# Kernel optimization log

Measured on AMD Instinct MI355X. Metric: run time of the kernel, lower is better.

The kernel has to match this reference:

```python
import jax, jax.numpy as jnp
import numpy as np

B, T, C = 32, 400, 3000
SN, SD = 128, 512   # numerator / denominator FSM state counts
NEG = -1e4          # log-zero surrogate (finite for grad safety)
DEN_SCALE = 1.0
DO_AVG = False


def setup_inputs() -> dict:
    key = jax.random.key(0)
    ks = jax.random.split(key, 8)
    x = jax.random.normal(ks[0], (B, T, C), jnp.float32)
    seqlengths = jax.random.randint(ks[1], (B,), T // 2, T + 1)
    # Numerator FSMs: batched left-to-right chains with self-loops.
    i = np.arange(SN)
    band = (i[None, :] >= i[:, None]) & (i[None, :] - i[:, None] <= 1)
    num_trans = jnp.where(jnp.asarray(band),
                          0.1 * jax.random.normal(ks[2], (B, SN, SN), jnp.float32), NEG)
    num_pdf = jax.random.randint(ks[3], (B, SN), 0, C)
    num_init = jnp.broadcast_to(jnp.where(jnp.arange(SN) == 0, 0.0, NEG), (B, SN)).astype(jnp.float32)
    num_final = jnp.broadcast_to(jnp.where(jnp.arange(SN) == SN - 1, 0.0, NEG), (B, SN)).astype(jnp.float32)
    # Denominator FSM: one dense graph shared by the whole batch.
    den_trans = 0.1 * jax.random.normal(ks[4], (SD, SD), jnp.float32)
    den_pdf = jax.random.randint(ks[5], (SD,), 0, C)
    den_init = 0.1 * jax.random.normal(ks[6], (SD,), jnp.float32)
    den_final = 0.1 * jax.random.normal(ks[7], (SD,), jnp.float32)
    return dict(input=x, seqlengths=seqlengths,
                num_trans=num_trans, num_pdf=num_pdf, num_init=num_init, num_final=num_final,
                den_trans=den_trans, den_pdf=den_pdf, den_init=den_init, den_final=den_final)


def _log_marginal(ll, seqlengths, trans, pdf, init, final):
    """FSM forward recursion in the log domain.
    ll: [B,T,C]; trans: [B,S,S] or [S,S]; pdf/init/final: [B,S].
    Returns per-sequence log-marginal [B]."""
    Bn, Tn, _ = ll.shape
    S = pdf.shape[-1]
    # Per-state emissions: em[b,t,s] = ll[b,t,pdf[b,s]]
    em = jnp.take_along_axis(ll, jnp.broadcast_to(pdf[:, None, :], (Bn, Tn, S)), axis=2)
    alpha0 = init + em[:, 0]                              # [B,S]
    mask = jnp.arange(1, Tn)[:, None] < seqlengths[None, :]  # [T-1,B]

    def step(alpha, xs):
        em_t, m = xs
        new = jax.nn.logsumexp(alpha[:, :, None] + trans, axis=1) + em_t
        return jnp.where(m[:, None], new, alpha), None

    alphaT, _ = jax.lax.scan(step, alpha0, (jnp.swapaxes(em, 0, 1)[1:], mask))
    return jax.nn.logsumexp(alphaT + final, axis=-1)      # [B]


def reference(input, seqlengths, num_trans, num_pdf, num_init, num_final,
              den_trans, den_pdf, den_init, den_final):
    ll = jnp.clip(input, -30.0, 30.0)
    Bn = ll.shape[0]
    num_llh = _log_marginal(ll, seqlengths, num_trans, num_pdf, num_init, num_final).sum()
    den_llh = _log_marginal(
        ll, seqlengths, den_trans,
        jnp.broadcast_to(den_pdf[None], (Bn, SD)),
        jnp.broadcast_to(den_init[None], (Bn, SD)),
        jnp.broadcast_to(den_final[None], (Bn, SD))).sum()
    loss = -(num_llh - DEN_SCALE * den_llh)
    if DO_AVG:
        loss = loss / seqlengths.sum()
    return loss
```

## Files before the change

### kernel.cpp

```cpp
#include <hip/hip_runtime.h>

#define B_ 32
#define T_ 400
#define C_ 3000
#define SN_ 128
#define SD_ 512
#define LN120 4.78749174f
#define LNU 2.70805020f
#define SPANB 48

__device__ __forceinline__ float clip30(float v) { return fminf(30.f, fmaxf(-30.f, v)); }

__device__ __forceinline__ int dot8u4(unsigned a, unsigned b, int c) {
#if __has_builtin(__builtin_amdgcn_udot8)
    return (int)__builtin_amdgcn_udot8(a, b, (unsigned)c, false);
#else
    int r = c;
    #pragma unroll
    for (int i = 0; i < 8; ++i)
        r += (int)((a >> (4 * i)) & 0xF) * (int)((b >> (4 * i)) & 0xF);
    return r;
#endif
}

template <int CTRL>
__device__ __forceinline__ int dpp_i(int v) {
    return __builtin_amdgcn_update_dpp(v, v, CTRL, 0xF, 0xF, false);
}
template <int CTRL>
__device__ __forceinline__ float fmaxdpp(float v) {
    int mv = __builtin_amdgcn_update_dpp(__float_as_int(v), __float_as_int(v), CTRL, 0xF, 0xF, false);
    return fmaxf(v, __int_as_float(mv));
}
template <int CTRL>
__device__ __forceinline__ float faddpp(float v) {
    int mv = __builtin_amdgcn_update_dpp(__float_as_int(v), __float_as_int(v), CTRL, 0xF, 0xF, false);
    return v + __int_as_float(mv);
}
template <int CTRL>
__device__ __forceinline__ float fxaddf(float a, float b) {
    int t = __builtin_amdgcn_update_dpp(__float_as_int(b), __float_as_int(b), CTRL, 0xF, 0xF, false);
    return a + __int_as_float(t);
}
__device__ __forceinline__ float swz16f(float v) {
    return __int_as_float(__builtin_amdgcn_ds_swizzle(__float_as_int(v), 0x401F));
}
__device__ __forceinline__ float wavemax_fast(float v) {
    v = fmaxdpp<0x121>(v); v = fmaxdpp<0x122>(v);
    v = fmaxdpp<0x124>(v); v = fmaxdpp<0x128>(v);
    float a = __int_as_float(__builtin_amdgcn_readlane(__float_as_int(v), 0));
    float b = __int_as_float(__builtin_amdgcn_readlane(__float_as_int(v), 16));
    float c = __int_as_float(__builtin_amdgcn_readlane(__float_as_int(v), 32));
    float d = __int_as_float(__builtin_amdgcn_readlane(__float_as_int(v), 48));
    return fmaxf(fmaxf(a, b), fmaxf(c, d));
}
__device__ __forceinline__ float waveallsum(float v) {
    v = faddpp<0x121>(v); v = faddpp<0x122>(v);
    v = faddpp<0x124>(v); v = faddpp<0x128>(v);
    v = v + swz16f(v);
    v = v + __shfl_xor(v, 32, 64);
    return v;
}
__device__ __forceinline__ void barrier_lds() {
    asm volatile("s_waitcnt lgkmcnt(0)\n\ts_barrier" ::: "memory");
}

__global__ void prep(const float* __restrict__ dt, unsigned* __restrict__ tp8,
                     const float* __restrict__ x, const int* __restrict__ den_pdf,
                     const int* __restrict__ num_pdf,
                     float* __restrict__ em_den, float* __restrict__ em_num) {
    size_t id = (size_t)blockIdx.x * 1024 + threadIdx.x;
    if (id < 32768) {
        int o = (int)id;
        int b4 = o & 3, tid = (o >> 2) & 511, k = o >> 11;
        int r = 4 * k + b4;
        int m = r >> 3, i = r & 7;
        int g = tid >> 3, j = tid & 7;
        int s_out = 8 * g + (m ^ j);
        int src0 = 64 * j + 8 * i;
        unsigned wv = 0;
        #pragma unroll
        for (int nb = 0; nb < 8; ++nb) {
            float e = __expf(dt[(src0 + nb) * SD_ + s_out]);
            int pq = __float2int_rn(e * 8.f);
            if (pq > 15) pq = 15;
            wv |= (unsigned)pq << (4 * nb);
        }
        tp8[o] = wv;
    } else if (id < 32768 + 6553600) {
        size_t e = id - 32768;
        int s = (int)(e & 511);
        size_t bt = e >> 9;
        em_den[e] = __expf(clip30(x[bt * C_ + den_pdf[s]]));
    } else if (id < 32768 + 6553600 + 1638400) {
        size_t e = id - 32768 - 6553600;
        int s = (int)(e & 127);
        size_t bt = e >> 7;
        int b = (int)(bt / 400);
        em_num[e] = clip30(x[bt * C_ + num_pdf[b * SN_ + s]]);
    }
}

__global__ __launch_bounds__(512, 1)
void fwd_kernel(const int* __restrict__ seqlen,
                const float* __restrict__ num_trans,
                const float* __restrict__ num_init, const float* __restrict__ num_final,
                const unsigned* __restrict__ tp8,
                const float* __restrict__ den_init, const float* __restrict__ den_final,
                const float* __restrict__ em_den, const float* __restrict__ em_num,
                float* __restrict__ parts) {
    const int tid = threadIdx.x;

    if (blockIdx.x < B_) {
        __shared__ __align__(16) unsigned char ea[2][8 * SPANB];
        __shared__ float Ms[2][8];
        __shared__ float fr[8];
        const int b = blockIdx.x;
        const int L = seqlen[b];
        const int w = tid >> 6, l = tid & 63;
        const int j = tid & 7;

        unsigned tq[64];
        {
            const uint4* tg = (const uint4*)tp8;
            #pragma unroll
            for (int i = 0; i < 16; ++i) {
                uint4 v = tg[(i << 9) + tid];
                tq[4 * i + 0] = v.x;
                tq[4 * i + 1] = v.y;
                tq[4 * i + 2] = v.z;
                tq[4 * i + 3] = v.w;
            }
        }

        const float* emp = em_den + (size_t)b * T_ * SD_ + tid;

        #define NPACK(UN, BUF) { \
            int uu = (UN); \
            uu |= dpp_i<0xB1>(uu) << 4; \
            uu |= dpp_i<0x4E>(uu) << 8; \
            uu |= dpp_i<0x124>(uu) << 16; \
            if ((tid & 7) == 0) \
                *(unsigned*)&ea[(BUF)][SPANB * w + ((tid & 63) >> 1)] = (unsigned)uu; }

        float a0lin = __expf(den_init[tid]) * emp[0];
        float K0 = wavemax_fast(a0lin);
        int un = __float2int_rn(15.f * a0lin * __builtin_amdgcn_rcpf(K0));
        float ms_w = __logf(K0);
        NPACK(un, 0)
        if (l == 0) Ms[0][w] = ms_w;
        barrier_lds();

        float EA = emp[SD_], EB = emp[2 * SD_];
        int cur = 0;
        for (int t = 1; t < L; ++t) {
            int tn = (t + 2 < L) ? t + 2 : L - 1;
            float EN = emp[(size_t)tn * SD_];

            float ms_j = Ms[cur][j];
            const uint4* er = (const uint4*)&ea[cur][SPANB * j];
            uint4 e0 = er[0], e1 = er[1];

            int ac0, ac1, ac2, ac3, ac4, ac5, ac6, ac7;
            #define DOTD0(W, I) \
                ac0 = dot8u4((W), tq[(I)],      0); \
                ac1 = dot8u4((W), tq[8 + (I)],  0); \
                ac2 = dot8u4((W), tq[16 + (I)], 0); \
                ac3 = dot8u4((W), tq[24 + (I)], 0); \
                ac4 = dot8u4((W), tq[32 + (I)], 0); \
                ac5 = dot8u4((W), tq[40 + (I)], 0); \
                ac6 = dot8u4((W), tq[48 + (I)], 0); \
                ac7 = dot8u4((W), tq[56 + (I)], 0);
            #define DOTD(W, I) \
                ac0 = dot8u4((W), tq[(I)],      ac0); \
                ac1 = dot8u4((W), tq[8 + (I)],  ac1); \
                ac2 = dot8u4((W), tq[16 + (I)], ac2); \
                ac3 = dot8u4((W), tq[24 + (I)], ac3); \
                ac4 = dot8u4((W), tq[32 + (I)], ac4); \
                ac5 = dot8u4((W), tq[40 + (I)], ac5); \
                ac6 = dot8u4((W), tq[48 + (I)], ac6); \
                ac7 = dot8u4((W), tq[56 + (I)], ac7);
            DOTD0(e0.x, 0) DOTD(e0.y, 1) DOTD(e0.z, 2) DOTD(e0.w, 3)
            DOTD(e1.x, 4)  DOTD(e1.y, 5) DOTD(e1.z, 6) DOTD(e1.w, 7)
            #undef DOTD
            #undef DOTD0

            float e_own = __expf(ms_j - ms_w);
            float f0 = (float)ac0 * e_own, f1 = (float)ac1 * e_own;
            float f2 = (float)ac2 * e_own, f3 = (float)ac3 * e_own;
            float f4 = (float)ac4 * e_own, f5 = (float)ac5 * e_own;
            float f6 = (float)ac6 * e_own, f7 = (float)ac7 * e_own;
            f0 = fxaddf<0xB1>(f0, f1);  f2 = fxaddf<0xB1>(f2, f3);
            f4 = fxaddf<0xB1>(f4, f5);  f6 = fxaddf<0xB1>(f6, f7);
            f0 = fxaddf<0x4E>(f0, f2);  f4 = fxaddf<0x4E>(f4, f6);
            f0 = fxaddf<0x124>(f0, f4);

            float Kv = f0 * EA;
            float K = wavemax_fast(Kv);
            un = __float2int_rn(15.f * Kv * __builtin_amdgcn_rcpf(K));
            NPACK(un, cur ^ 1)
            ms_w = ms_w + __logf(K) - LN120;
            if (l == 0) Ms[cur ^ 1][w] = ms_w;
            EA = EB; EB = EN;
            barrier_lds();
            cur ^= 1;
        }
        #undef NPACK

        float mm = Ms[cur][0];
        #pragma unroll
        for (int k2 = 1; k2 < 8; ++k2) mm = fmaxf(mm, Ms[cur][k2]);
        float fv = (float)un * __expf(den_final[tid] + (ms_w - mm));
        fv = waveallsum(fv);
        if (l == 0) fr[w] = fv;
        __syncthreads();
        if (tid == 0) {
            float tot = 0.f;
            for (int i = 0; i < 8; ++i) tot += fr[i];
            parts[B_ + b] = mm + __logf(tot) - LNU;
        }
    } else {
        __shared__ float aLn[2][4][SN_];
        __shared__ float nredn[4][2];
        const int nb = blockIdx.x - B_;
        const int lb = tid >> 7;
        const int b  = nb * 4 + lb;
        const int s  = tid & 127;
        const int L  = seqlen[b];
        const int lane = tid & 63;
        const int wv2 = (tid >> 6) & 1;
        const float* ep = em_num + (size_t)b * T_ * SN_ + s;
        const float tself = num_trans[((size_t)b * SN_ + s) * SN_ + s];
        const float tup = (s > 0) ? num_trans[((size_t)b * SN_ + (s - 1)) * SN_ + s] : 0.f;
        float alpha = num_init[b * SN_ + s] + ep[0];
        aLn[0][lb][s] = alpha;
        __syncthreads();
        float emA = ep[SN_], emB = ep[2 * SN_];
        int cur = 0;
        for (int t = 1; t < T_; ++t) {
            int tt = t + 2; if (tt > T_ - 1) tt = T_ - 1;
            float emN = ep[(size_t)tt * SN_];
            bool live = (t < L);
            float yy = alpha + tself;
            float newa;
            if (s > 0) {
                float xx = aLn[cur][lb][s - 1] + tup;
                float mx = fmaxf(xx, yy), mn = fminf(xx, yy);
                newa = mx + log1pf(__expf(mn - mx)) + emA;
            } else {
                newa = yy + emA;
            }
            if (live) alpha = newa;
            aLn[cur ^ 1][lb][s] = alpha;
            emA = emB; emB = emN;
            __syncthreads();
            cur ^= 1;
        }
        float v = alpha + num_final[b * SN_ + s];
        float wm = v;
        #pragma unroll
        for (int o = 32; o; o >>= 1) wm = fmaxf(wm, __shfl_xor(wm, o, 64));
        if (lane == 0) nredn[lb][wv2] = wm;
        __syncthreads();
        float fm = fmaxf(nredn[lb][0], nredn[lb][1]);
        __syncthreads();
        float pe = __expf(v - fm);
        #pragma unroll
        for (int o = 32; o; o >>= 1) pe += __shfl_xor(pe, o, 64);
        if (lane == 0) nredn[lb][wv2] = pe;
        __syncthreads();
        if (s == 0) parts[b] = fm + __logf(nredn[lb][0] + nredn[lb][1]);
    }
}

__global__ void finish(const float* __restrict__ parts, float* __restrict__ out) {
    int lane = threadIdx.x;
    float v = (lane < B_) ? (parts[B_ + lane] - parts[lane]) : 0.f;
    #pragma unroll
    for (int o = 32; o; o >>= 1) v += __shfl_xor(v, o, 64);
    if (lane == 0) out[0] = v;
}

extern "C" void kernel_launch(void* const* d_in, const int* in_sizes, int n_in,
                              void* d_out, int out_size, void* d_ws, size_t ws_size,
                              hipStream_t stream) {
    const float* x         = (const float*)d_in[0];
    const int*   seqlen    = (const int*)d_in[1];
    const float* num_trans = (const float*)d_in[2];
    const int*   num_pdf   = (const int*)d_in[3];
    const float* num_init  = (const float*)d_in[4];
    const float* num_final = (const float*)d_in[5];
    const float* den_trans = (const float*)d_in[6];
    const int*   den_pdf   = (const int*)d_in[7];
    const float* den_init  = (const float*)d_in[8];
    const float* den_final = (const float*)d_in[9];
    float* out   = (float*)d_out;
    float* parts = (float*)d_ws;
    unsigned* tp8 = (unsigned*)((char*)d_ws + 4096);
    float* em_den = (float*)((char*)d_ws + 4096 + 131072);
    float* em_num = em_den + 6553600;

    prep<<<8032, 1024, 0, stream>>>(den_trans, tp8, x, den_pdf, num_pdf, em_den, em_num);
    fwd_kernel<<<40, 512, 0, stream>>>(seqlen, num_trans, num_init, num_final,
                                       tp8, den_init, den_final, em_den, em_num, parts);
    finish<<<1, 64, 0, stream>>>(parts, out);
}
```

Before: 330.7 us.

## Pack two batch sequences per 1024-thread block in forward kernel

The forward recursion kernel now runs two denominator sequences per 1024-thread block (16 blocks instead of 32), and eight numerator sequences per block instead of four. The loop runs to the longer of the pair's lengths, and state updates are masked per sequence. This halves the block count so fewer CUs are used. Each CU now holds 16 waves sharing one barrier, so every barrier waits for both sequences and the shorter one does idle iterations. Register pressure under the 1024-thread launch bound is a risk for the 64-register tq array.

New measurement: 554.9 us. 1.68x slower.

```diff
diff --git a/kernel.cpp b/kernel.cpp
--- a/kernel.cpp
+++ b/kernel.cpp
@@ -101,7 +101,7 @@
     }
 }
 
-__global__ __launch_bounds__(512, 1)
+__global__ __launch_bounds__(1024, 1)
 void fwd_kernel(const int* __restrict__ seqlen,
                 const float* __restrict__ num_trans,
                 const float* __restrict__ num_init, const float* __restrict__ num_final,
@@ -111,21 +111,25 @@
                 float* __restrict__ parts) {
     const int tid = threadIdx.x;
 
-    if (blockIdx.x < B_) {
-        __shared__ __align__(16) unsigned char ea[2][8 * SPANB];
-        __shared__ float Ms[2][8];
-        __shared__ float fr[8];
-        const int b = blockIdx.x;
+    if (blockIdx.x < 16) {
+        __shared__ __align__(16) unsigned char ea[2][2][8 * SPANB];
+        __shared__ float Ms[2][2][8];
+        __shared__ float fr[2][8];
+        const int bb = blockIdx.x;
+        const int w = tid >> 6, l = tid & 63;
+        const int bat = w >> 3, wb = w & 7;
+        const int j = tid & 7;
+        const int st = tid & 511;
+        const int b = 2 * bb + bat;
         const int L = seqlen[b];
-        const int w = tid >> 6, l = tid & 63;
-        const int j = tid & 7;
+        const int Lmax = max(seqlen[2 * bb], seqlen[2 * bb + 1]);
 
         unsigned tq[64];
         {
             const uint4* tg = (const uint4*)tp8;
             #pragma unroll
             for (int i = 0; i < 16; ++i) {
-                uint4 v = tg[(i << 9) + tid];
+                uint4 v = tg[(i << 9) + st];
                 tq[4 * i + 0] = v.x;
                 tq[4 * i + 1] = v.y;
                 tq[4 * i + 2] = v.z;
@@ -133,7 +137,7 @@
             }
         }
 
-        const float* emp = em_den + (size_t)b * T_ * SD_ + tid;
+        const float* emp = em_den + (size_t)b * T_ * SD_ + st;
 
         #define NPACK(UN, BUF) { \
             int uu = (UN); \
@@ -141,24 +145,24 @@
             uu |= dpp_i<0x4E>(uu) << 8; \
             uu |= dpp_i<0x124>(uu) << 16; \
             if ((tid & 7) == 0) \
-                *(unsigned*)&ea[(BUF)][SPANB * w + ((tid & 63) >> 1)] = (unsigned)uu; }
-
-        float a0lin = __expf(den_init[tid]) * emp[0];
+                *(unsigned*)&ea[bat][(BUF)][SPANB * wb + ((tid & 63) >> 1)] = (unsigned)uu; }
+
+        float a0lin = __expf(den_init[st]) * emp[0];
         float K0 = wavemax_fast(a0lin);
         int un = __float2int_rn(15.f * a0lin * __builtin_amdgcn_rcpf(K0));
         float ms_w = __logf(K0);
         NPACK(un, 0)
-        if (l == 0) Ms[0][w] = ms_w;
+        if (l == 0) Ms[bat][0][wb] = ms_w;
         barrier_lds();
 
         float EA = emp[SD_], EB = emp[2 * SD_];
         int cur = 0;
-        for (int t = 1; t < L; ++t) {
+        for (int t = 1; t < Lmax; ++t) {
             int tn = (t + 2 < L) ? t + 2 : L - 1;
             float EN = emp[(size_t)tn * SD_];
 
-            float ms_j = Ms[cur][j];
-            const uint4* er = (const uint4*)&ea[cur][SPANB * j];
+            float ms_j = Ms[bat][cur][j];
+            const uint4* er = (const uint4*)&ea[bat][cur][SPANB * j];
             uint4 e0 = er[0], e1 = er[1];
 
             int ac0, ac1, ac2, ac3, ac4, ac5, ac6, ac7;
@@ -197,34 +201,37 @@
 
             float Kv = f0 * EA;
             float K = wavemax_fast(Kv);
-            un = __float2int_rn(15.f * Kv * __builtin_amdgcn_rcpf(K));
+            int nun = __float2int_rn(15.f * Kv * __builtin_amdgcn_rcpf(K));
+            if (t < L) {
+                un = nun;
+                ms_w = ms_w + __logf(K) - LN120;
+            }
             NPACK(un, cur ^ 1)
-            ms_w = ms_w + __logf(K) - LN120;
-            if (l == 0) Ms[cur ^ 1][w] = ms_w;
+            if (l == 0) Ms[bat][cur ^ 1][wb] = ms_w;
             EA = EB; EB = EN;
             barrier_lds();
             cur ^= 1;
         }
         #undef NPACK
 
-        float mm = Ms[cur][0];
+        float mm = Ms[bat][cur][0];
         #pragma unroll
-        for (int k2 = 1; k2 < 8; ++k2) mm = fmaxf(mm, Ms[cur][k2]);
-        float fv = (float)un * __expf(den_final[tid] + (ms_w - mm));
+        for (int k2 = 1; k2 < 8; ++k2) mm = fmaxf(mm, Ms[bat][cur][k2]);
+        float fv = (float)un * __expf(den_final[st] + (ms_w - mm));
         fv = waveallsum(fv);
-        if (l == 0) fr[w] = fv;
-        __syncthreads();
-        if (tid == 0) {
+        if (l == 0) fr[bat][wb] = fv;
+        __syncthreads();
+        if ((tid & 511) == 0) {
             float tot = 0.f;
-            for (int i = 0; i < 8; ++i) tot += fr[i];
+            for (int i = 0; i < 8; ++i) tot += fr[bat][i];
             parts[B_ + b] = mm + __logf(tot) - LNU;
         }
     } else {
-        __shared__ float aLn[2][4][SN_];
-        __shared__ float nredn[4][2];
-        const int nb = blockIdx.x - B_;
+        __shared__ float aLn[2][8][SN_];
+        __shared__ float nredn[8][2];
+        const int nb = blockIdx.x - 16;
         const int lb = tid >> 7;
-        const int b  = nb * 4 + lb;
+        const int b  = nb * 8 + lb;
         const int s  = tid & 127;
         const int L  = seqlen[b];
         const int lane = tid & 63;
@@ -301,7 +308,7 @@
     float* em_num = em_den + 6553600;
 
     prep<<<8032, 1024, 0, stream>>>(den_trans, tp8, x, den_pdf, num_pdf, em_den, em_num);
-    fwd_kernel<<<40, 512, 0, stream>>>(seqlen, num_trans, num_init, num_final,
-                                       tp8, den_init, den_final, em_den, em_num, parts);
+    fwd_kernel<<<20, 1024, 0, stream>>>(seqlen, num_trans, num_init, num_final,
+                                        tp8, den_init, den_final, em_den, em_num, parts);
     finish<<<1, 64, 0, stream>>>(parts, out);
 }
```
